# Kernel tuning notes

Hardware: AMD Instinct MI355X
Metric: run time of the kernel (lower is better)

## Reference

```python
import jax, jax.numpy as jnp
import numpy as np

B, T = 256, 32
CNN_DIM, HW = 512, 14
HID, V = 8, 37


def setup_inputs() -> dict:
    key = jax.random.key(0)
    ks = jax.random.split(key, 10)
    s = 0.1  # param init scale
    return {
        "features": jax.random.normal(ks[0], (B, CNN_DIM, HW, HW), jnp.float32),
        "captions": jax.random.uniform(ks[1], (B, T, V), jnp.float32),
        "W_ih": jax.random.normal(ks[2], (4 * HID, V), jnp.float32) * s,
        "b_ih": jax.random.normal(ks[3], (4 * HID,), jnp.float32) * s,
        "W_hh": jax.random.normal(ks[4], (4 * HID, HID), jnp.float32) * s,
        "b_hh": jax.random.normal(ks[5], (4 * HID,), jnp.float32) * s,
        "W_in": jax.random.normal(ks[6], (V, CNN_DIM), jnp.float32) * s,
        "b_in": jax.random.normal(ks[7], (V,), jnp.float32) * s,
        "W_out": jax.random.normal(ks[8], (V, HID), jnp.float32) * s,
        "b_out": jax.random.normal(ks[9], (V,), jnp.float32) * s,
        "isTraining": 1,
    }


def _lstm_step(h, c, x, W_ih, b_ih, W_hh, b_hh):
    # PyTorch LSTMCell gate order: i, f, g, o
    gates = x @ W_ih.T + b_ih + h @ W_hh.T + b_hh  # [B, 4*HID]
    i, f, g, o = jnp.split(gates, 4, axis=1)
    c = jax.nn.sigmoid(f) * c + jax.nn.sigmoid(i) * jnp.tanh(g)
    h = jax.nn.sigmoid(o) * jnp.tanh(c)
    return h, c


def reference(features, captions, W_ih, b_ih, W_hh, b_hh, W_in, b_in, W_out, b_out, isTraining):
    bsz, seq_len, vocab = captions.shape
    hid = W_hh.shape[1]
    # AdaptiveAvgPool2d(1) + flatten + fc_in
    pooled = features.mean(axis=(2, 3))          # [B, cnn_dim]
    x0 = pooled @ W_in.T + b_in                  # [B, V]
    h0 = jnp.zeros((bsz, hid), features.dtype)
    c0 = jnp.zeros((bsz, hid), features.dtype)

    if isTraining:
        # teacher forcing: inputs are [x0, captions[:,0], ..., captions[:,T-2]]
        xs = jnp.concatenate([x0[:, None, :], captions[:, : seq_len - 1, :]], axis=1)

        def step(carry, x):
            h, c = carry
            h, c = _lstm_step(h, c, x, W_ih, b_ih, W_hh, b_hh)
            out = h @ W_out.T + b_out
            return (h, c), out

        _, outs = jax.lax.scan(step, (h0, c0), jnp.swapaxes(xs, 0, 1))
        outputs = jnp.swapaxes(outs, 0, 1)       # [B, T, V]
    else:
        # greedy feedback: feed previous (pre-softmax) fc_out logits
        h, c = _lstm_step(h0, c0, x0, W_ih, b_ih, W_hh, b_hh)
        out0 = h @ W_out.T + b_out

        def step(carry, _):
            h, c, prev = carry
            h, c = _lstm_step(h, c, prev, W_ih, b_ih, W_hh, b_hh)
            out = h @ W_out.T + b_out
            return (h, c, out), out

        _, outs = jax.lax.scan(step, (h, c, out0), None, length=seq_len - 1)
        outputs = jnp.concatenate([out0[:, None, :], jnp.swapaxes(outs, 0, 1)], axis=1)

    # Faithful to original: Softmax(dim=1) is over the TIME axis
    return jax.nn.softmax(outputs, axis=1)
```

## Files before the change

kernel.cpp:

```cpp
#include <hip/hip_runtime.h>
#include <math.h>


#define BDIM 512

__device__ __forceinline__ float wave_reduce_sum(float v) {
#pragma unroll
    for (int off = 32; off; off >>= 1) v += __shfl_down(v, off, 64);
    return v;
}

__device__ __forceinline__ float sigf(float x) { return 1.0f / (1.0f + __expf(-x)); }
__device__ __forceinline__ float tanhfast(float x) { return 1.0f - 2.0f / (__expf(2.0f * x) + 1.0f); }

__global__ void pool_kernel(
    const float* __restrict__ features, float* __restrict__ pooled )
{
    constexpr int NPIX = 196;
    const int wid  = (blockIdx.x << 4) + (threadIdx.x >> 6);
    const int lane = threadIdx.x & 63;
    const float* base = features + (size_t)wid * NPIX;

    float s = 0.0f;
    if (lane < 49) {
        const float4 v = ((const float4*)base)[lane];
        s = (v.x + v.y) + (v.z + v.w);
    }
    s = wave_reduce_sum(s);
    if (lane == 0) pooled[wid] = s * (1.0f / 196.0f);
}

__global__ __launch_bounds__(BDIM) void lstm_rest(
    const float* __restrict__ pooled_g, const float* __restrict__ captions,
    const float* __restrict__ W_ih, const float* __restrict__ b_ih,
    const float* __restrict__ W_hh, const float* __restrict__ b_hh,
    const float* __restrict__ W_in, const float* __restrict__ b_in,
    const float* __restrict__ W_out, const float* __restrict__ b_out,
    const int* __restrict__ isTraining, float* __restrict__ out)
{
    constexpr int T = 32, V = 37, HID = 8, C = 512, G = 32;

    __shared__ float pooled[C];
    __shared__ float xs[T * V];
    __shared__ float wih[G * V];
    __shared__ float xg[T * G];
    __shared__ float hist[T * HID];
    __shared__ float lg[T * V];
    __shared__ float bsum[G];
    __shared__ float inv_s[V];

    const int b    = blockIdx.x;
    const int tid  = threadIdx.x;
    const int lane = tid & 63;
    const int w    = tid >> 6;

    pooled[tid] = pooled_g[(size_t)b * C + tid];
    for (int i = tid; i < G * V; i += BDIM) wih[i] = W_ih[i];
    for (int i = tid + V; i < T * V; i += BDIM) xs[i] = captions[(size_t)b * T * V + (i - V)];
    if (tid < G) bsum[tid] = b_ih[tid] + b_hh[tid];
    __syncthreads();

    for (int v = w; v < V; v += 8) {
        const float* wr = W_in + (size_t)v * C;
        float p = 0.0f;
#pragma unroll
        for (int k = 0; k < 8; ++k) p += pooled[lane + 64 * k] * wr[lane + 64 * k];
        p = wave_reduce_sum(p);
        if (lane == 0) xs[v] = p + b_in[v];
    }
    __syncthreads();

    for (int e = tid; e < T * G; e += BDIM) {
        const int t = e >> 5, j = e & 31;
        const float* xr = xs + t * V;
        const float* wr = wih + j * V;
        float acc = bsum[j];
#pragma unroll
        for (int v = 0; v < V; ++v) acc += xr[v] * wr[v];
        xg[e] = acc;
    }
    __syncthreads();

    const bool train = (isTraining[0] != 0);
    if (w == 0) {
        const int j = lane & 31;
        const int k8 = lane & 7;
        float whh_r[HID];
#pragma unroll
        for (int k = 0; k < HID; ++k) whh_r[k] = W_hh[j * HID + k];
        float wout_r[HID];
        float bout_r = 0.0f;
        if (lane < V) {
#pragma unroll
            for (int k = 0; k < HID; ++k) wout_r[k] = W_out[lane * HID + k];
            bout_r = b_out[lane];
        }
        float h = 0.0f, c = 0.0f;
        float prevout = 0.0f;

        for (int t = 0; t < T; ++t) {
            float gate;
            if (train || t == 0) {
                gate = xg[t * G + j];
            } else {
                float acc = bsum[j];
                const float* wr = wih + j * V;
#pragma unroll
                for (int v = 0; v < V; ++v) acc += __shfl(prevout, v, 64) * wr[v];
                gate = acc;
            }
#pragma unroll
            for (int k = 0; k < HID; ++k) gate += __shfl(h, k, 64) * whh_r[k];

            const int sec = lane >> 3;
            const float a = (sec == 2) ? tanhfast(gate) : sigf(gate);

            const float ig = __shfl(a, k8, 64);
            const float fg = __shfl(a, 8 + k8, 64);
            const float gg = __shfl(a, 16 + k8, 64);
            const float og = __shfl(a, 24 + k8, 64);
            c = fg * c + ig * gg;
            h = og * tanhfast(c);

            if (train) {
                if (lane < HID) hist[t * HID + lane] = h;
            } else {
                float o = bout_r;
#pragma unroll
                for (int k = 0; k < HID; ++k) o += __shfl(h, k, 64) * wout_r[k];
                if (lane < V) lg[t * V + lane] = o;
                prevout = o;
            }
        }
    }
    __syncthreads();

    if (train) {
        for (int e = tid; e < T * V; e += BDIM) {
            const int t = e / V, v = e - t * V;
            const float* hr = hist + t * HID;
            const float* wr = W_out + v * HID;
            float acc = b_out[v];
#pragma unroll
            for (int k = 0; k < HID; ++k) acc += hr[k] * wr[k];
            lg[e] = acc;
        }
    }
    __syncthreads();

    if (tid < V) {
        float m = -1e30f;
#pragma unroll
        for (int t = 0; t < T; ++t) m = fmaxf(m, lg[t * V + tid]);
        float s = 0.0f;
#pragma unroll
        for (int t = 0; t < T; ++t) {
            const float e = __expf(lg[t * V + tid] - m);
            lg[t * V + tid] = e;
            s += e;
        }
        inv_s[tid] = 1.0f / s;
    }
    __syncthreads();

    float* outB = out + (size_t)b * T * V;
    for (int e = tid; e < T * V; e += BDIM) {
        const int t = e / V, v = e - t * V;
        outB[e] = lg[e] * inv_s[v];
    }
}

extern "C" void kernel_launch(void* const* d_in, const int* in_sizes, int n_in,
                              void* d_out, int out_size, void* d_ws, size_t ws_size,
                              hipStream_t stream) {
    const float* features = (const float*)d_in[0];
    const float* captions = (const float*)d_in[1];
    const float* W_ih     = (const float*)d_in[2];
    const float* b_ih     = (const float*)d_in[3];
    const float* W_hh     = (const float*)d_in[4];
    const float* b_hh     = (const float*)d_in[5];
    const float* W_in     = (const float*)d_in[6];
    const float* b_in     = (const float*)d_in[7];
    const float* W_out    = (const float*)d_in[8];
    const float* b_out    = (const float*)d_in[9];
    const int*   isTrain  = (const int*)d_in[10];
    float* out = (float*)d_out;

    float* pooled = (float*)d_ws;

    pool_kernel<<<8192, 1024, 0, stream>>>(features, pooled);
    lstm_rest<<<256, BDIM, 0, stream>>>(pooled, captions, W_ih, b_ih, W_hh, b_hh,
                                        W_in, b_in, W_out, b_out, isTrain, out);
}
```

Baseline: 185.2 us.

## Remap pooling so each 8-lane group reduces one channel with 7 float4 loads

The pooling kernel is restructured so each wave handles 8 channels per iteration: 7 lanes per group each load 7 float4s, then reduce with 8-wide shuffles. Each wave loops over 4 channel batches, and the grid shrinks from 8192x1024 to 1024x256 threads. The aim is to raise memory-level parallelism per lane, avoid wasting 15 of 64 lanes per channel, and cut launch and block overhead. The trade-off is a strided per-lane access pattern with 112-byte lane strides, which may coalesce less well, plus fewer total waves in flight to hide latency.

```diff
diff --git a/kernel.cpp b/kernel.cpp
--- a/kernel.cpp
+++ b/kernel.cpp
@@ -13,21 +13,35 @@
 __device__ __forceinline__ float sigf(float x) { return 1.0f / (1.0f + __expf(-x)); }
 __device__ __forceinline__ float tanhfast(float x) { return 1.0f - 2.0f / (__expf(2.0f * x) + 1.0f); }
 
-__global__ void pool_kernel(
+__global__ __launch_bounds__(256) void pool_kernel(
     const float* __restrict__ features, float* __restrict__ pooled )
 {
-    constexpr int NPIX = 196;
-    const int wid  = (blockIdx.x << 4) + (threadIdx.x >> 6);
-    const int lane = threadIdx.x & 63;
-    const float* base = features + (size_t)wid * NPIX;
-
-    float s = 0.0f;
-    if (lane < 49) {
-        const float4 v = ((const float4*)base)[lane];
-        s = (v.x + v.y) + (v.z + v.w);
-    }
-    s = wave_reduce_sum(s);
-    if (lane == 0) pooled[wid] = s * (1.0f / 196.0f);
+    const int wglobal = (blockIdx.x << 2) + (threadIdx.x >> 6);
+    const int lane    = threadIdx.x & 63;
+    const int g       = lane >> 3;
+    const int k7      = lane & 7;
+
+    for (int i = 0; i < 4; ++i) {
+        const int ch = (i << 15) + (wglobal << 3) + g;
+        const float4* p = (const float4*)features + (size_t)ch * 49 + k7 * 7;
+        float s = 0.0f;
+        if (k7 < 7) {
+            float4 v0 = p[0], v1 = p[1], v2 = p[2], v3 = p[3],
+                   v4 = p[4], v5 = p[5], v6 = p[6];
+            float a0 = (v0.x + v0.y) + (v0.z + v0.w);
+            float a1 = (v1.x + v1.y) + (v1.z + v1.w);
+            float a2 = (v2.x + v2.y) + (v2.z + v2.w);
+            float a3 = (v3.x + v3.y) + (v3.z + v3.w);
+            float a4 = (v4.x + v4.y) + (v4.z + v4.w);
+            float a5 = (v5.x + v5.y) + (v5.z + v5.w);
+            float a6 = (v6.x + v6.y) + (v6.z + v6.w);
+            s = ((a0 + a1) + (a2 + a3)) + ((a4 + a5) + a6);
+        }
+        s += __shfl_down(s, 4, 8);
+        s += __shfl_down(s, 2, 8);
+        s += __shfl_down(s, 1, 8);
+        if (k7 == 0) pooled[ch] = s * (1.0f / 196.0f);
+    }
 }
 
 __global__ __launch_bounds__(BDIM) void lstm_rest(
@@ -188,7 +202,7 @@
 
     float* pooled = (float*)d_ws;
 
-    pool_kernel<<<8192, 1024, 0, stream>>>(features, pooled);
+    pool_kernel<<<1024, 256, 0, stream>>>(features, pooled);
     lstm_rest<<<256, BDIM, 0, stream>>>(pooled, captions, W_ih, b_ih, W_hh, b_hh,
                                         W_in, b_in, W_out, b_out, isTrain, out);
 }
```

Measured after the change: 186.5 us. No clear change (+0.7%).
